# Kernel tuning notes

Measured on AMD Instinct MI355X. Metric: run time of the kernel, lower is better.

Reference implementation:

```python
import jax, jax.numpy as jnp
import numpy as np

N_NODES = 50000
N_EDGES = 800000
F_IN = 128
HID = 32
HEADS = 8
N_CLS = 2
NEG_SLOPE = 0.2


def _segment_softmax(logits, seg, num_segments):
    # logits: [E, H], seg: [E] destination indices
    m = jax.ops.segment_max(logits, seg, num_segments=num_segments)  # [N, H]
    m = jnp.where(jnp.isfinite(m), m, 0.0)
    e = jnp.exp(logits - m[seg])
    s = jax.ops.segment_sum(e, seg, num_segments=num_segments)  # [N, H]
    return e / (s[seg] + 1e-16)


def _gat_conv(x, src, dst, W, a_src, a_dst, bias, heads, out_ch, concat):
    N = x.shape[0]
    h = (x @ W).reshape(N, heads, out_ch)           # [N, H, C]
    alpha_src = jnp.einsum('nhc,hc->nh', h, a_src)  # [N, H]
    alpha_dst = jnp.einsum('nhc,hc->nh', h, a_dst)  # [N, H]
    logits = jax.nn.leaky_relu(alpha_src[src] + alpha_dst[dst], NEG_SLOPE)  # [E, H]
    alpha = _segment_softmax(logits, dst, N)        # [E, H]
    msg = h[src] * alpha[:, :, None]                # [E, H, C]
    out = jax.ops.segment_sum(msg, dst, num_segments=N)  # [N, H, C]
    out = out.reshape(N, heads * out_ch) if concat else out.mean(axis=1)
    return out + bias


def setup_inputs() -> dict:
    key = jax.random.key(0)
    ks = jax.random.split(key, 12)
    x = jax.random.normal(ks[0], (N_NODES, F_IN), dtype=jnp.float32)
    edge_index = jax.random.randint(ks[1], (2, N_EDGES), 0, N_NODES, dtype=jnp.int32)
    batch = jnp.zeros((N_NODES,), dtype=jnp.int32)
    g1 = 1.0 / np.sqrt(F_IN)
    g2 = 1.0 / np.sqrt(HEADS * HID)
    W1 = jax.random.normal(ks[2], (F_IN, HEADS * HID), dtype=jnp.float32) * g1
    a1_src = jax.random.normal(ks[3], (HEADS, HID), dtype=jnp.float32) * g2
    a1_dst = jax.random.normal(ks[4], (HEADS, HID), dtype=jnp.float32) * g2
    b1 = jnp.zeros((HEADS * HID,), dtype=jnp.float32)
    W2 = jax.random.normal(ks[5], (HEADS * HID, N_CLS), dtype=jnp.float32) * g2
    a2_src = jax.random.normal(ks[6], (1, N_CLS), dtype=jnp.float32)
    a2_dst = jax.random.normal(ks[7], (1, N_CLS), dtype=jnp.float32)
    b2 = jnp.zeros((N_CLS,), dtype=jnp.float32)
    return {"x": x, "edge_index": edge_index, "batch": batch,
            "W1": W1, "a1_src": a1_src, "a1_dst": a1_dst, "b1": b1,
            "W2": W2, "a2_src": a2_src, "a2_dst": a2_dst, "b2": b2}


def reference(x, edge_index, batch, W1, a1_src, a1_dst, b1, W2, a2_src, a2_dst, b2):
    N = x.shape[0]
    # PyG GATConv default add_self_loops=True
    loops = jnp.arange(N, dtype=edge_index.dtype)
    src = jnp.concatenate([edge_index[0], loops])
    dst = jnp.concatenate([edge_index[1], loops])
    # dropout layers are no-ops at inference (training=False)
    h = _gat_conv(x, src, dst, W1, a1_src, a1_dst, b1, HEADS, HID, concat=True)
    h = jax.nn.elu(h)
    out = _gat_conv(h, src, dst, W2, a2_src, a2_dst, b2, 1, N_CLS, concat=False)
    return out
```

## Files before the change

kernel.cpp:

```cpp
#include <hip/hip_runtime.h>

#define NN 50000
#define NP 50048
#define NE 800000
#define ET (NE + NN)
#define NB 196
#define CAP 8192
#define P1_B ((ET + 1023) / 1024)
#define CONVW_B 128
#define CONVX_B (NP * 32 / 256)
#define CONV_B (CONVW_B + CONVX_B)
#define GEMM_B (NP / 64)

typedef __attribute__((ext_vector_type(8))) short short8;
typedef __attribute__((ext_vector_type(4))) float f32x4;

static __device__ __forceinline__ float bf2f(unsigned short u) {
  union { unsigned int i; float f; } v; v.i = ((unsigned int)u) << 16; return v.f;
}
static __device__ __forceinline__ unsigned short f2bf(float f) {
  union { unsigned int i; float f; } v; v.f = f;
  unsigned int r = v.i + 0x7fffu + ((v.i >> 16) & 1u);
  return (unsigned short)(r >> 16);
}
static __device__ __forceinline__ float lrelu(float z) { return z > 0.f ? z : 0.2f * z; }

__global__ void k_conv(const float* __restrict__ W1, unsigned short* __restrict__ wh,
                       const float* __restrict__ x, unsigned short* __restrict__ xh) {
  const int b = blockIdx.x;
  const int tid = threadIdx.x;
  if (b < CONVW_B) {
    int i = b * 256 + tid;
    int k = i >> 8, n = i & 255;
    wh[n * 128 + k] = f2bf(W1[i]);
  } else {
    int i4 = (b - CONVW_B) * 256 + tid;
    int i = i4 * 4;
    int row = i >> 7;
    float4 v = (row < NN) ? *(const float4*)(x + i) : (float4){0.f, 0.f, 0.f, 0.f};
    ushort4 h;
    h.x = f2bf(v.x);
    h.y = f2bf(v.y);
    h.z = f2bf(v.z);
    h.w = f2bf(v.w);
    *(ushort4*)(xh + i) = h;
  }
}

__global__ __launch_bounds__(1024) void k_p1(const int* __restrict__ ei,
                                             int* __restrict__ gcount,
                                             int* __restrict__ tmp) {
  __shared__ int hist[NB];
  __shared__ int lbase[NB];
  const int tid = threadIdx.x;
  if (tid < NB) hist[tid] = 0;
  __syncthreads();
  int e = blockIdx.x * 1024 + tid;
  bool valid = (e < ET);
  int src = 0, dst = 0, b = 0, loc = 0;
  if (valid) {
    src = (e < NE) ? ei[e] : (e - NE);
    dst = (e < NE) ? ei[NE + e] : (e - NE);
    b = dst >> 8;
    loc = atomicAdd(&hist[b], 1);
  }
  __syncthreads();
  if (tid < NB) {
    int c = hist[tid];
    lbase[tid] = (c > 0) ? atomicAdd(&gcount[tid], c) : 0;
  }
  __syncthreads();
  if (valid) tmp[b * CAP + lbase[b] + loc] = (src << 8) | (dst & 255);
}

__global__ __launch_bounds__(1024) void k_p2(const int* __restrict__ tmp,
                                             const int* __restrict__ gcount,
                                             int* __restrict__ ssrc,
                                             int* __restrict__ row_ptr) {
  __shared__ int hist[256];
  __shared__ int sa[256];
  __shared__ int sb[256];
  __shared__ int cur[256];
  __shared__ int base_sh;
  const int t = threadIdx.x;
  const int b = blockIdx.x;
  const int n_b = gcount[b];
  if (t < 256) sa[t] = (t < NB) ? gcount[t] : 0;
  __syncthreads();
  {
    int* s = sa;
    int* d = sb;
    for (int off = 1; off < 256; off <<= 1) {
      if (t < 256) {
        int v = s[t];
        if (t >= off) v += s[t - off];
        d[t] = v;
      }
      int* tm = s; s = d; d = tm;
      __syncthreads();
    }
    if (t == 0) {
      base_sh = (b == 0) ? 0 : s[b - 1];
      if (b == 0) row_ptr[NN] = ET;
    }
  }
  if (t < 256) hist[t] = 0;
  __syncthreads();
  const int base = base_sh;
  for (int i = t; i < n_b; i += 1024) {
    int p = tmp[b * CAP + i];
    atomicAdd(&hist[p & 255], 1);
  }
  __syncthreads();
  if (t < 256) sa[t] = hist[t];
  __syncthreads();
  {
    int* s = sa;
    int* d = sb;
    for (int off = 1; off < 256; off <<= 1) {
      if (t < 256) {
        int v = s[t];
        if (t >= off) v += s[t - off];
        d[t] = v;
      }
      int* tm = s; s = d; d = tm;
      __syncthreads();
    }
    if (t < 256) {
      int excl = (t == 0) ? 0 : s[t - 1];
      int start = base + excl;
      cur[t] = start;
      int d_glob = (b << 8) + t;
      if (d_glob < NN) row_ptr[d_glob] = start;
    }
  }
  __syncthreads();
  for (int i = t; i < n_b; i += 1024) {
    int p = tmp[b * CAP + i];
    int bin = p & 255;
    int pos = atomicAdd(&cur[bin], 1);
    ssrc[pos] = p >> 8;
  }
}

__global__ __launch_bounds__(256) void k_gemm1(
    const unsigned short* __restrict__ xh, const unsigned short* __restrict__ wh,
    const float* __restrict__ a1s, const float* __restrict__ a1d,
    unsigned short* __restrict__ h1, float* __restrict__ as1, float* __restrict__ ad1) {
  __shared__ unsigned short hst[64][264];
  const int tid = threadIdx.x;
  const int w = tid >> 6, lane = tid & 63;
  const int quad = lane >> 4, m16 = lane & 15;
  const int row0 = blockIdx.x * 64;
  const int koff = quad * 8;

  f32x4 acc[4][4];
  for (int mt = 0; mt < 4; ++mt)
    for (int nt = 0; nt < 4; ++nt) acc[mt][nt] = (f32x4){0.f, 0.f, 0.f, 0.f};

  for (int kt = 0; kt < 4; ++kt) {
    short8 ah[4], bh[4];
    for (int mt = 0; mt < 4; ++mt) {
      size_t ra = (size_t)(row0 + mt * 16 + m16) * 128 + kt * 32 + koff;
      ah[mt] = *(const short8*)(xh + ra);
    }
    for (int nt = 0; nt < 4; ++nt) {
      size_t rb = (size_t)(w * 64 + nt * 16 + m16) * 128 + kt * 32 + koff;
      bh[nt] = *(const short8*)(wh + rb);
    }
    for (int mt = 0; mt < 4; ++mt)
      for (int nt = 0; nt < 4; ++nt)
        acc[mt][nt] = __builtin_amdgcn_mfma_f32_16x16x32_bf16(ah[mt], bh[nt], acc[mt][nt], 0, 0, 0);
  }
  for (int mt = 0; mt < 4; ++mt)
    for (int nt = 0; nt < 4; ++nt) {
      int c = w * 64 + nt * 16 + m16;
      int rb = mt * 16 + quad * 4;
      for (int r = 0; r < 4; ++r) hst[rb + r][c] = f2bf(acc[mt][nt][r]);
    }
  __syncthreads();
  for (int p = 0; p < 8; ++p) {
    int idx = p * 256 + tid;
    int row = idx >> 5, u4 = idx & 31;
    int grow = row0 + row;
    if (grow < NN) {
      uint4 v = *(const uint4*)&hst[row][u4 * 8];
      *(uint4*)(h1 + (size_t)grow * 256 + u4 * 8) = v;
    }
  }
  for (int p = 0; p < 2; ++p) {
    int id = p * 256 + tid;
    int row = id >> 3, head = id & 7;
    int grow = row0 + row;
    if (grow < NN) {
      float sa = 0.f, sd = 0.f;
      for (int c = 0; c < 32; ++c) {
        float hv = bf2f(hst[row][head * 32 + c]);
        sa = fmaf(hv, a1s[head * 32 + c], sa);
        sd = fmaf(hv, a1d[head * 32 + c], sd);
      }
      as1[(size_t)grow * 8 + head] = sa;
      ad1[(size_t)grow * 8 + head] = sd;
    }
  }
}

__global__ __launch_bounds__(256) void k_agg1(
    const int* __restrict__ row_ptr, const int* __restrict__ ssrc,
    const unsigned short* __restrict__ h1, const float* __restrict__ as1,
    const float* __restrict__ ad1, const float* __restrict__ b1,
    const float* __restrict__ W2, const float* __restrict__ a2s,
    const float* __restrict__ a2d, float4* __restrict__ nd) {
  const int lane = threadIdx.x & 63;
  const int dst = (int)((blockIdx.x * blockDim.x + threadIdx.x) >> 6);
  if (dst >= NN) return;
  const int start = row_ptr[dst], end = row_ptr[dst + 1];
  const int hA = lane & 7;
  const int eoff = lane >> 3;
  const int hB = lane >> 3;
  const int cB = (lane & 7) * 4;
  const float ad_h = ad1[(size_t)dst * 8 + hA];
  float s_loc = 0.f;
  float acc0 = 0.f, acc1 = 0.f, acc2 = 0.f, acc3 = 0.f;
  for (int base = start; base < end; base += 16) {
    int ea = base + eoff, eb = base + 8 + eoff;
    int sa_ = 0, sb_ = 0;
    float wa = 0.f, wb = 0.f;
    if (ea < end) {
      sa_ = ssrc[ea];
      wa = __expf(lrelu(as1[(size_t)sa_ * 8 + hA] + ad_h));
    }
    if (eb < end) {
      sb_ = ssrc[eb];
      wb = __expf(lrelu(as1[(size_t)sb_ * 8 + hA] + ad_h));
    }
    s_loc += wa + wb;
    uint2 u[16];
    float w16[16];
#pragma unroll
    for (int j = 0; j < 8; ++j) {
      int se = __shfl(sa_, j * 8);
      w16[j] = __shfl(wa, j * 8 + hB);
      u[j] = *(const uint2*)(h1 + (size_t)se * 256 + hB * 32 + cB);
    }
#pragma unroll
    for (int j = 0; j < 8; ++j) {
      int se = __shfl(sb_, j * 8);
      w16[8 + j] = __shfl(wb, j * 8 + hB);
      u[8 + j] = *(const uint2*)(h1 + (size_t)se * 256 + hB * 32 + cB);
    }
#pragma unroll
    for (int j = 0; j < 16; ++j) {
      float w = w16[j];
      acc0 = fmaf(w, bf2f((unsigned short)(u[j].x & 0xffffu)), acc0);
      acc1 = fmaf(w, bf2f((unsigned short)(u[j].x >> 16)), acc1);
      acc2 = fmaf(w, bf2f((unsigned short)(u[j].y & 0xffffu)), acc2);
      acc3 = fmaf(w, bf2f((unsigned short)(u[j].y >> 16)), acc3);
    }
  }
  s_loc += __shfl_xor(s_loc, 8);
  s_loc += __shfl_xor(s_loc, 16);
  s_loc += __shfl_xor(s_loc, 32);
  const float inv_s = 1.f / (s_loc + 1e-16f);
  const float inv_sB = __shfl(inv_s, hB);
  acc0 *= inv_sB; acc1 *= inv_sB; acc2 *= inv_sB; acc3 *= inv_sB;
  const int col = hB * 32 + cB;
  float av[4] = {acc0, acc1, acc2, acc3};
  float tp0 = 0.f, tp1 = 0.f;
  for (int j = 0; j < 4; ++j) {
    float v = av[j] + b1[col + j];
    v = v > 0.f ? v : (__expf(v) - 1.f);
    tp0 = fmaf(v, W2[(col + j) * 2 + 0], tp0);
    tp1 = fmaf(v, W2[(col + j) * 2 + 1], tp1);
  }
  for (int off = 32; off >= 1; off >>= 1) {
    tp0 += __shfl_xor(tp0, off);
    tp1 += __shfl_xor(tp1, off);
  }
  if (lane == 0) {
    float s2v = tp0 * a2s[0] + tp1 * a2s[1];
    float d2v = tp0 * a2d[0] + tp1 * a2d[1];
    nd[dst] = (float4){tp0, tp1, s2v, d2v};
  }
}

__global__ __launch_bounds__(256) void k_agg2(
    const int* __restrict__ row_ptr, const int* __restrict__ ssrc,
    const float4* __restrict__ nd, const float* __restrict__ b2,
    float* __restrict__ out) {
  int gid = blockIdx.x * 256 + threadIdx.x;
  int n = gid >> 3;
  int l8 = threadIdx.x & 7;
  if (n >= NN) return;
  int st = row_ptr[n], en = row_ptr[n + 1];
  float dv = nd[n].w;
  float ssum = 0.f, o0 = 0.f, o1 = 0.f;
  for (int e = st + l8; e < en; e += 8) {
    int s = ssrc[e];
    float4 v = nd[s];
    float w = __expf(lrelu(v.z + dv));
    ssum += w;
    o0 = fmaf(w, v.x, o0);
    o1 = fmaf(w, v.y, o1);
  }
  ssum += __shfl_xor(ssum, 1); o0 += __shfl_xor(o0, 1); o1 += __shfl_xor(o1, 1);
  ssum += __shfl_xor(ssum, 2); o0 += __shfl_xor(o0, 2); o1 += __shfl_xor(o1, 2);
  ssum += __shfl_xor(ssum, 4); o0 += __shfl_xor(o0, 4); o1 += __shfl_xor(o1, 4);
  if (l8 == 0) {
    float inv = 1.f / (ssum + 1e-16f);
    out[(size_t)n * 2 + 0] = o0 * inv + b2[0];
    out[(size_t)n * 2 + 1] = o1 * inv + b2[1];
  }
}

extern "C" void kernel_launch(void* const* d_in, const int* in_sizes, int n_in,
                              void* d_out, int out_size, void* d_ws, size_t ws_size,
                              hipStream_t stream) {
  const float* x = (const float*)d_in[0];
  const int* ei = (const int*)d_in[1];
  const float* W1 = (const float*)d_in[3];
  const float* a1s = (const float*)d_in[4];
  const float* a1d = (const float*)d_in[5];
  const float* b1 = (const float*)d_in[6];
  const float* W2 = (const float*)d_in[7];
  const float* a2s = (const float*)d_in[8];
  const float* a2d = (const float*)d_in[9];
  const float* b2 = (const float*)d_in[10];
  float* out = (float*)d_out;

  char* ws = (char*)d_ws;
  size_t off = 0;
  auto alloc = [&](size_t bytes) -> void* {
    void* p = ws + off;
    off += (bytes + 255) & ~(size_t)255;
    return p;
  };
  int* gcount = (int*)alloc((size_t)NB * 4);
  int* tmp = (int*)alloc((size_t)NB * CAP * 4);
  int* row_ptr = (int*)alloc((size_t)(NN + 1) * 4);
  int* ssrc = (int*)alloc((size_t)ET * 4);
  unsigned short* xh = (unsigned short*)alloc((size_t)NP * 128 * 2);
  unsigned short* wh = (unsigned short*)alloc((size_t)32768 * 2);
  unsigned short* h1 = (unsigned short*)alloc((size_t)NN * 256 * 2);
  float* as1 = (float*)alloc((size_t)NN * 8 * 4);
  float* ad1 = (float*)alloc((size_t)NN * 8 * 4);
  float4* nd = (float4*)alloc((size_t)NN * 16);
  (void)ws_size; (void)in_sizes; (void)n_in; (void)out_size;

  hipMemsetAsync(gcount, 0, (size_t)NB * 4, stream);
  k_conv<<<CONV_B, 256, 0, stream>>>(W1, wh, x, xh);
  k_p1<<<P1_B, 1024, 0, stream>>>(ei, gcount, tmp);
  k_p2<<<NB, 1024, 0, stream>>>(tmp, gcount, ssrc, row_ptr);
  k_gemm1<<<GEMM_B, 256, 0, stream>>>(xh, wh, a1s, a1d, h1, as1, ad1);
  k_agg1<<<(NN + 3) / 4, 256, 0, stream>>>(row_ptr, ssrc, h1, as1, ad1, b1, W2, a2s, a2d, nd);
  k_agg2<<<(NN * 8 + 255) / 256, 256, 0, stream>>>(row_ptr, ssrc, nd, b2, out);
}
```

Before: 226.2 us.

## Merge independent preprocessing kernels into two block-partitioned launches

Four kernels are folded into two. The bf16 conversion and the edge bucketing pass now share one launch of 1024-thread blocks, and the CSR finalize pass and the first GEMM share a second launch, with each block choosing its role from blockIdx. The aim is to cut launch overhead and let independent work run at the same time on the GPU. In exchange, the CSR pass now runs with 256 threads per block instead of 1024 and reuses the GEMM's shared-memory buffer.

```diff
diff --git a/kernel.cpp b/kernel.cpp
--- a/kernel.cpp
+++ b/kernel.cpp
@@ -7,10 +7,11 @@
 #define NB 196
 #define CAP 8192
 #define P1_B ((ET + 1023) / 1024)
-#define CONVW_B 128
-#define CONVX_B (NP * 32 / 256)
-#define CONV_B (CONVW_B + CONVX_B)
+#define CONVW_B 32
+#define CONVX_B (NP * 32 / 1024)
+#define FRONT_B (P1_B + CONVW_B + CONVX_B)
 #define GEMM_B (NP / 64)
+#define MID_B (NB + GEMM_B)
 
 typedef __attribute__((ext_vector_type(8))) short short8;
 typedef __attribute__((ext_vector_type(4))) float f32x4;
@@ -25,16 +26,39 @@
 }
 static __device__ __forceinline__ float lrelu(float z) { return z > 0.f ? z : 0.2f * z; }
 
-__global__ void k_conv(const float* __restrict__ W1, unsigned short* __restrict__ wh,
-                       const float* __restrict__ x, unsigned short* __restrict__ xh) {
+__global__ __launch_bounds__(1024) void k_front(
+    const int* __restrict__ ei, int* __restrict__ gcount, int* __restrict__ tmp,
+    const float* __restrict__ W1, unsigned short* __restrict__ wh,
+    const float* __restrict__ x, unsigned short* __restrict__ xh) {
+  __shared__ int hist[NB];
+  __shared__ int lbase[NB];
   const int b = blockIdx.x;
   const int tid = threadIdx.x;
-  if (b < CONVW_B) {
-    int i = b * 256 + tid;
+  if (b < P1_B) {
+    if (tid < NB) hist[tid] = 0;
+    __syncthreads();
+    int e = b * 1024 + tid;
+    bool valid = (e < ET);
+    int src = 0, dst = 0, bk = 0, loc = 0;
+    if (valid) {
+      src = (e < NE) ? ei[e] : (e - NE);
+      dst = (e < NE) ? ei[NE + e] : (e - NE);
+      bk = dst >> 8;
+      loc = atomicAdd(&hist[bk], 1);
+    }
+    __syncthreads();
+    if (tid < NB) {
+      int c = hist[tid];
+      lbase[tid] = (c > 0) ? atomicAdd(&gcount[tid], c) : 0;
+    }
+    __syncthreads();
+    if (valid) tmp[bk * CAP + lbase[bk] + loc] = (src << 8) | (dst & 255);
+  } else if (b < P1_B + CONVW_B) {
+    int i = (b - P1_B) * 1024 + tid;
     int k = i >> 8, n = i & 255;
     wh[n * 128 + k] = f2bf(W1[i]);
   } else {
-    int i4 = (b - CONVW_B) * 256 + tid;
+    int i4 = (b - P1_B - CONVW_B) * 1024 + tid;
     int i = i4 * 4;
     int row = i >> 7;
     float4 v = (row < NN) ? *(const float4*)(x + i) : (float4){0.f, 0.f, 0.f, 0.f};
@@ -47,111 +71,78 @@
   }
 }
 
-__global__ __launch_bounds__(1024) void k_p1(const int* __restrict__ ei,
-                                             int* __restrict__ gcount,
-                                             int* __restrict__ tmp) {
-  __shared__ int hist[NB];
-  __shared__ int lbase[NB];
+__global__ __launch_bounds__(256) void k_mid(
+    const int* __restrict__ tmp, const int* __restrict__ gcount,
+    int* __restrict__ ssrc, int* __restrict__ row_ptr,
+    const unsigned short* __restrict__ xh, const unsigned short* __restrict__ wh,
+    const float* __restrict__ a1s, const float* __restrict__ a1d,
+    unsigned short* __restrict__ h1, float* __restrict__ as1, float* __restrict__ ad1) {
+  __shared__ unsigned short hst[64][264];
   const int tid = threadIdx.x;
-  if (tid < NB) hist[tid] = 0;
-  __syncthreads();
-  int e = blockIdx.x * 1024 + tid;
-  bool valid = (e < ET);
-  int src = 0, dst = 0, b = 0, loc = 0;
-  if (valid) {
-    src = (e < NE) ? ei[e] : (e - NE);
-    dst = (e < NE) ? ei[NE + e] : (e - NE);
-    b = dst >> 8;
-    loc = atomicAdd(&hist[b], 1);
-  }
-  __syncthreads();
-  if (tid < NB) {
-    int c = hist[tid];
-    lbase[tid] = (c > 0) ? atomicAdd(&gcount[tid], c) : 0;
-  }
-  __syncthreads();
-  if (valid) tmp[b * CAP + lbase[b] + loc] = (src << 8) | (dst & 255);
-}
-
-__global__ __launch_bounds__(1024) void k_p2(const int* __restrict__ tmp,
-                                             const int* __restrict__ gcount,
-                                             int* __restrict__ ssrc,
-                                             int* __restrict__ row_ptr) {
-  __shared__ int hist[256];
-  __shared__ int sa[256];
-  __shared__ int sb[256];
-  __shared__ int cur[256];
-  __shared__ int base_sh;
-  const int t = threadIdx.x;
-  const int b = blockIdx.x;
-  const int n_b = gcount[b];
-  if (t < 256) sa[t] = (t < NB) ? gcount[t] : 0;
-  __syncthreads();
-  {
-    int* s = sa;
-    int* d = sb;
-    for (int off = 1; off < 256; off <<= 1) {
-      if (t < 256) {
+  if (blockIdx.x < NB) {
+    int* hist = (int*)&hst[0][0];
+    int* sa = hist + 256;
+    int* sb = sa + 256;
+    int* cur = sb + 256;
+    int* base_sh = cur + 256;
+    const int t = tid;
+    const int b = blockIdx.x;
+    const int n_b = gcount[b];
+    sa[t] = (t < NB) ? gcount[t] : 0;
+    __syncthreads();
+    {
+      int* s = sa;
+      int* d = sb;
+      for (int off = 1; off < 256; off <<= 1) {
         int v = s[t];
         if (t >= off) v += s[t - off];
         d[t] = v;
+        int* tm = s; s = d; d = tm;
+        __syncthreads();
       }
-      int* tm = s; s = d; d = tm;
-      __syncthreads();
-    }
-    if (t == 0) {
-      base_sh = (b == 0) ? 0 : s[b - 1];
-      if (b == 0) row_ptr[NN] = ET;
-    }
-  }
-  if (t < 256) hist[t] = 0;
-  __syncthreads();
-  const int base = base_sh;
-  for (int i = t; i < n_b; i += 1024) {
-    int p = tmp[b * CAP + i];
-    atomicAdd(&hist[p & 255], 1);
-  }
-  __syncthreads();
-  if (t < 256) sa[t] = hist[t];
-  __syncthreads();
-  {
-    int* s = sa;
-    int* d = sb;
-    for (int off = 1; off < 256; off <<= 1) {
-      if (t < 256) {
+      if (t == 0) {
+        base_sh[0] = (b == 0) ? 0 : s[b - 1];
+        if (b == 0) row_ptr[NN] = ET;
+      }
+    }
+    hist[t] = 0;
+    __syncthreads();
+    const int base = base_sh[0];
+    for (int i = t; i < n_b; i += 256) {
+      int p = tmp[b * CAP + i];
+      atomicAdd(&hist[p & 255], 1);
+    }
+    __syncthreads();
+    sa[t] = hist[t];
+    __syncthreads();
+    {
+      int* s = sa;
+      int* d = sb;
+      for (int off = 1; off < 256; off <<= 1) {
         int v = s[t];
         if (t >= off) v += s[t - off];
         d[t] = v;
+        int* tm = s; s = d; d = tm;
+        __syncthreads();
       }
-      int* tm = s; s = d; d = tm;
-      __syncthreads();
-    }
-    if (t < 256) {
       int excl = (t == 0) ? 0 : s[t - 1];
       int start = base + excl;
       cur[t] = start;
       int d_glob = (b << 8) + t;
       if (d_glob < NN) row_ptr[d_glob] = start;
     }
-  }
-  __syncthreads();
-  for (int i = t; i < n_b; i += 1024) {
-    int p = tmp[b * CAP + i];
-    int bin = p & 255;
-    int pos = atomicAdd(&cur[bin], 1);
-    ssrc[pos] = p >> 8;
-  }
-}
-
-__global__ __launch_bounds__(256) void k_gemm1(
-    const unsigned short* __restrict__ xh, const unsigned short* __restrict__ wh,
-    const float* __restrict__ a1s, const float* __restrict__ a1d,
-    unsigned short* __restrict__ h1, float* __restrict__ as1, float* __restrict__ ad1) {
-  __shared__ unsigned short hst[64][264];
-  const int tid = threadIdx.x;
+    __syncthreads();
+    for (int i = t; i < n_b; i += 256) {
+      int p = tmp[b * CAP + i];
+      int pos = atomicAdd(&cur[p & 255], 1);
+      ssrc[pos] = p >> 8;
+    }
+    return;
+  }
+  const int gb = blockIdx.x - NB;
   const int w = tid >> 6, lane = tid & 63;
   const int quad = lane >> 4, m16 = lane & 15;
-  const int row0 = blockIdx.x * 64;
+  const int row0 = gb * 64;
   const int koff = quad * 8;
 
   f32x4 acc[4][4];
@@ -348,10 +339,8 @@
   (void)ws_size; (void)in_sizes; (void)n_in; (void)out_size;
 
   hipMemsetAsync(gcount, 0, (size_t)NB * 4, stream);
-  k_conv<<<CONV_B, 256, 0, stream>>>(W1, wh, x, xh);
-  k_p1<<<P1_B, 1024, 0, stream>>>(ei, gcount, tmp);
-  k_p2<<<NB, 1024, 0, stream>>>(tmp, gcount, ssrc, row_ptr);
-  k_gemm1<<<GEMM_B, 256, 0, stream>>>(xh, wh, a1s, a1d, h1, as1, ad1);
+  k_front<<<FRONT_B, 1024, 0, stream>>>(ei, gcount, tmp, W1, wh, x, xh);
+  k_mid<<<MID_B, 256, 0, stream>>>(tmp, gcount, ssrc, row_ptr, xh, wh, a1s, a1d, h1, as1, ad1);
   k_agg1<<<(NN + 3) / 4, 256, 0, stream>>>(row_ptr, ssrc, h1, as1, ad1, b1, W2, a2s, a2d, nd);
   k_agg2<<<(NN * 8 + 255) / 256, 256, 0, stream>>>(row_ptr, ssrc, nd, b2, out);
 }
```

New measurement: 216.1 us. -4.5%, faster.
